# Kernel tuning notes

Measured on AMD Instinct MI355X. Metric: run time of the kernel, lower is better.

The kernel has to match this reference:

```python
import jax, jax.numpy as jnp
import numpy as np

N_NODES = 100000
N_EDGES = 800000
F_IN, N_HID, N_CLS = 256, 128, 40


def setup_inputs() -> dict:
    key = jax.random.key(0)
    ks = jax.random.split(key, 6)
    features = jax.random.normal(ks[0], (N_NODES, F_IN), dtype=jnp.float32)
    src = jax.random.randint(ks[1], (N_EDGES,), 0, N_NODES, dtype=jnp.int64)
    dst = jax.random.randint(ks[2], (N_EDGES,), 0, N_NODES, dtype=jnp.int64)
    W1 = jax.random.normal(ks[3], (F_IN, N_HID), dtype=jnp.float32) / np.sqrt(F_IN)
    b1 = jnp.zeros((N_HID,), dtype=jnp.float32)
    W2 = jax.random.normal(ks[4], (N_HID, N_CLS), dtype=jnp.float32) / np.sqrt(N_HID)
    b2 = jnp.zeros((N_CLS,), dtype=jnp.float32)
    return {"features": features, "src": src, "dst": dst,
            "W1": W1, "b1": b1, "W2": W2, "b2": b2}


def reference(features, src, dst, W1, b1, W2, b2):
    # DGL GraphConv with norm='both': h = D_dst^{-1/2} A (D_src^{-1/2} x) W + b
    # Eval mode: dropout(p=0.85) is identity.
    N = features.shape[0]
    ones = jnp.ones(src.shape[0], dtype=features.dtype)
    out_deg = jax.ops.segment_sum(ones, src, num_segments=N)
    in_deg = jax.ops.segment_sum(ones, dst, num_segments=N)
    norm_src = jnp.where(out_deg > 0, out_deg ** -0.5, 0.0)[:, None]  # [N,1]
    norm_dst = jnp.where(in_deg > 0, in_deg ** -0.5, 0.0)[:, None]

    def gconv(x, W, b):
        # project first (in_feats >= out_feats here) to shrink SpMM width
        h = (x * norm_src) @ W                                # [N, out]
        agg = jax.ops.segment_sum(h[src], dst, num_segments=N)  # sparse aggregate
        return agg * norm_dst + b

    x = jax.nn.relu(gconv(features, W1, b1))
    return gconv(x, W2, b2)
```

## Files before the change

kernel.cpp:

```cpp
#include <hip/hip_runtime.h>
#include <hip/hip_bf16.h>
#include <math.h>


#define F_IN  256
#define F_HID 128
#define F_CLS 40

#define RSZ 8192
#define NSL 32

typedef __bf16 bf16_t;
typedef bf16_t bf16x8 __attribute__((ext_vector_type(8)));
typedef float floatx4 __attribute__((ext_vector_type(4)));

static __device__ __forceinline__ unsigned short f2b(float f) {
    __hip_bfloat16 h = __float2bfloat16(f);
    return __builtin_bit_cast(unsigned short, h);
}
static __device__ __forceinline__ float b2f(unsigned short u) {
    return __uint_as_float((unsigned)u << 16);
}
static __device__ __forceinline__ unsigned short f2h(float f) {
    return __builtin_bit_cast(unsigned short, (_Float16)f);
}
static __device__ __forceinline__ float h2f(unsigned short u) {
    return (float)__builtin_bit_cast(_Float16, u);
}

__global__ __launch_bounds__(256) void hist_kernel(
    const int* __restrict__ src, const int* __restrict__ dst,
    unsigned* __restrict__ partial_s, unsigned* __restrict__ partial_d, int E)
{
    __shared__ unsigned h[RSZ];
    const int t = threadIdx.x;
    const int r  = blockIdx.x / NSL;
    const int sl = blockIdx.x % NSL;
    const int lo = r * RSZ;
    const int* __restrict__ keys = blockIdx.y ? dst : src;
    unsigned* __restrict__ part = blockIdx.y ? partial_d : partial_s;

    for (int i = t; i < RSZ; i += 256) h[i] = 0;
    __syncthreads();

    const int slice = (E + NSL - 1) / NSL;
    const int e0 = sl * slice;
    const int e1 = min(E, e0 + slice);

    int e = e0 + t;
    for (; e + 7 * 256 < e1; e += 8 * 256) {
        int k[8];
        #pragma unroll
        for (int i = 0; i < 8; ++i) k[i] = keys[e + i * 256];
        #pragma unroll
        for (int i = 0; i < 8; ++i) {
            unsigned kk = (unsigned)(k[i] - lo);
            if (kk < RSZ) atomicAdd(&h[kk], 1u);
        }
    }
    for (; e < e1; e += 256) {
        unsigned kk = (unsigned)(keys[e] - lo);
        if (kk < RSZ) atomicAdd(&h[kk], 1u);
    }
    __syncthreads();

    unsigned* dst_p = part + (size_t)blockIdx.x * RSZ;
    for (int i = t; i < RSZ; i += 256) dst_p[i] = h[i];
}

__global__ __launch_bounds__(256) void degnorm_kernel(
    const unsigned* __restrict__ partial_s, const unsigned* __restrict__ partial_d,
    int* __restrict__ cnt_dst, float* __restrict__ norm_src,
    float* __restrict__ norm_dst, int N)
{
    int i = blockIdx.x * 256 + threadIdx.x;
    if (i >= N) return;
    int r = i / RSZ;
    int off = i & (RSZ - 1);
    const unsigned* ps = partial_s + (size_t)r * NSL * RSZ + off;
    const unsigned* pd = partial_d + (size_t)r * NSL * RSZ + off;
    unsigned ss = 0, sd = 0;
    #pragma unroll
    for (int sl = 0; sl < NSL; ++sl) {
        ss += ps[(size_t)sl * RSZ];
        sd += pd[(size_t)sl * RSZ];
    }
    cnt_dst[i] = (int)sd;
    norm_src[i] = ss ? 1.0f / sqrtf((float)ss) : 0.0f;
    norm_dst[i] = sd ? 1.0f / sqrtf((float)sd) : 0.0f;
}

__global__ __launch_bounds__(256) void scan1_kernel(const int* __restrict__ cnt,
                                                    int* __restrict__ row_off,
                                                    int* __restrict__ blk_sums, int N) {
    __shared__ int s[256];
    const int t = threadIdx.x;
    const int base = blockIdx.x * 1024 + t * 4;
    int v0 = (base + 0 < N) ? cnt[base + 0] : 0;
    int v1 = (base + 1 < N) ? cnt[base + 1] : 0;
    int v2 = (base + 2 < N) ? cnt[base + 2] : 0;
    int v3 = (base + 3 < N) ? cnt[base + 3] : 0;
    int local = v0 + v1 + v2 + v3;
    s[t] = local;
    __syncthreads();
    for (int off = 1; off < 256; off <<= 1) {
        int x = (t >= off) ? s[t - off] : 0;
        __syncthreads();
        s[t] += x;
        __syncthreads();
    }
    int excl = s[t] - local;
    if (t == 255) blk_sums[blockIdx.x] = s[t];
    if (base + 0 < N) row_off[base + 0] = excl;
    if (base + 1 < N) row_off[base + 1] = excl + v0;
    if (base + 2 < N) row_off[base + 2] = excl + v0 + v1;
    if (base + 3 < N) row_off[base + 3] = excl + v0 + v1 + v2;
}

__global__ __launch_bounds__(256) void scan2_kernel(int* __restrict__ blk_sums, int B) {
    __shared__ int s[256];
    const int t = threadIdx.x;
    int local = (t < B) ? blk_sums[t] : 0;
    s[t] = local;
    __syncthreads();
    for (int off = 1; off < 256; off <<= 1) {
        int x = (t >= off) ? s[t - off] : 0;
        __syncthreads();
        s[t] += x;
        __syncthreads();
    }
    if (t < B) blk_sums[t] = s[t] - local;
}

__global__ __launch_bounds__(256) void scan3_kernel(int* __restrict__ row_off,
                                                    const int* __restrict__ blk_sums,
                                                    int N, int E) {
    const int t = threadIdx.x;
    const int base = blockIdx.x * 1024 + t * 4;
    const int add = blk_sums[blockIdx.x];
    #pragma unroll
    for (int i = 0; i < 4; ++i) {
        int idx = base + i;
        if (idx < N) row_off[idx] += add;
    }
    if (blockIdx.x == 0 && t == 0) row_off[N] = E;
}

__global__ __launch_bounds__(256) void slicepref_kernel(
    unsigned* __restrict__ partial_d, const int* __restrict__ row_off,
    int N, int NRtot)
{
    int idx = blockIdx.x * 256 + threadIdx.x;
    if (idx >= NRtot) return;
    int r = idx / RSZ;
    int i = idx & (RSZ - 1);
    unsigned run = (idx < N) ? (unsigned)row_off[idx] : 0u;
    unsigned* p = partial_d + (size_t)r * NSL * RSZ + i;
    #pragma unroll
    for (int sl = 0; sl < NSL; ++sl) {
        unsigned c = p[(size_t)sl * RSZ];
        p[(size_t)sl * RSZ] = run;
        run += c;
    }
}

__global__ __launch_bounds__(256) void scatter2_kernel(
    const int* __restrict__ src, const int* __restrict__ dst,
    const unsigned* __restrict__ pref, int* __restrict__ csr_src, int E)
{
    __shared__ unsigned cur[RSZ];
    const int t = threadIdx.x;
    const int r  = blockIdx.x / NSL;
    const int sl = blockIdx.x % NSL;
    const int lo = r * RSZ;
    const unsigned* p = pref + (size_t)blockIdx.x * RSZ;

    for (int i = t; i < RSZ; i += 256) cur[i] = p[i];
    __syncthreads();

    const int slice = (E + NSL - 1) / NSL;
    const int e0 = sl * slice;
    const int e1 = min(E, e0 + slice);

    int e = e0 + t;
    for (; e + 7 * 256 < e1; e += 8 * 256) {
        int d[8], s[8];
        #pragma unroll
        for (int i = 0; i < 8; ++i) { d[i] = dst[e + i * 256]; s[i] = src[e + i * 256]; }
        #pragma unroll
        for (int i = 0; i < 8; ++i) {
            unsigned k = (unsigned)(d[i] - lo);
            if (k < RSZ) {
                unsigned pos = atomicAdd(&cur[k], 1u);
                csr_src[pos] = s[i];
            }
        }
    }
    for (; e < e1; e += 256) {
        unsigned k = (unsigned)(dst[e] - lo);
        if (k < RSZ) {
            unsigned pos = atomicAdd(&cur[k], 1u);
            csr_src[pos] = src[e];
        }
    }
}

__global__ __launch_bounds__(256) void pack_w1t_kernel(const float* __restrict__ W1,
                                                       __hip_bfloat16* __restrict__ W1t) {
    int idx = blockIdx.x * 256 + threadIdx.x;
    int n = idx >> 8;
    int k = idx & 255;
    W1t[idx] = __float2bfloat16(W1[(size_t)k * F_HID + n]);
}

__global__ __launch_bounds__(512, 4) void gemm1_mfma_kernel(
    const float* __restrict__ X, const __hip_bfloat16* __restrict__ W1t,
    const float* __restrict__ norm_src, __hip_bfloat16* __restrict__ h1b, int N)
{
    __shared__ __hip_bfloat16 Bs[128 * 256];
    const int t = threadIdx.x;
    const int node0 = blockIdx.x * 128;
    const int lane = t & 63;
    const int w = t >> 6;
    const int l15 = lane & 15;
    const int quad = lane >> 4;

    const int arow = node0 + w * 16 + l15;
    const bool valid = arow < N;
    const int arow_c = valid ? arow : (N - 1);
    const float ns = valid ? norm_src[arow] : 0.0f;

    const float* xp = X + (size_t)arow_c * F_IN + quad * 8;

    float4 araw[4];
    araw[0] = *(const float4*)(xp + 0);
    araw[1] = *(const float4*)(xp + 4);
    araw[2] = *(const float4*)(xp + 32);
    araw[3] = *(const float4*)(xp + 36);

    #pragma unroll
    for (int i = 0; i < 8; ++i) {
        int idx = i * 512 + t;
        int row = idx >> 5;
        int ch  = idx & 31;
        uint4 v = *(const uint4*)(W1t + (size_t)row * F_IN + ch * 8);
        int d = row * 256 + ((ch * 8) ^ ((row & 7) << 3));
        *(uint4*)(Bs + d) = v;
    }
    __syncthreads();

    const int swz = (l15 & 7) << 3;
    const int bbase0 = l15 * 256 + ((quad * 8) ^ swz);
    const int bbase1 = l15 * 256 + ((32 + quad * 8) ^ swz);

    floatx4 acc[8] = {};

    #pragma unroll
    for (int c = 0; c < 4; ++c) {
        bf16x8 ab0, ab1;
        {
            union { bf16x8 v; unsigned short u[8]; } cv;
            cv.u[0] = f2b(araw[0].x * ns); cv.u[1] = f2b(araw[0].y * ns);
            cv.u[2] = f2b(araw[0].z * ns); cv.u[3] = f2b(araw[0].w * ns);
            cv.u[4] = f2b(araw[1].x * ns); cv.u[5] = f2b(araw[1].y * ns);
            cv.u[6] = f2b(araw[1].z * ns); cv.u[7] = f2b(araw[1].w * ns);
            ab0 = cv.v;
            cv.u[0] = f2b(araw[2].x * ns); cv.u[1] = f2b(araw[2].y * ns);
            cv.u[2] = f2b(araw[2].z * ns); cv.u[3] = f2b(araw[2].w * ns);
            cv.u[4] = f2b(araw[3].x * ns); cv.u[5] = f2b(araw[3].y * ns);
            cv.u[6] = f2b(araw[3].z * ns); cv.u[7] = f2b(araw[3].w * ns);
            ab1 = cv.v;
        }
        if (c < 3) {
            araw[0] = *(const float4*)(xp + (c + 1) * 64 + 0);
            araw[1] = *(const float4*)(xp + (c + 1) * 64 + 4);
            araw[2] = *(const float4*)(xp + (c + 1) * 64 + 32);
            araw[3] = *(const float4*)(xp + (c + 1) * 64 + 36);
        }
        #pragma unroll
        for (int nt = 0; nt < 8; ++nt) {
            bf16x8 b = *(const bf16x8*)(Bs + bbase0 + nt * 16 * 256 + c * 64);
            acc[nt] = __builtin_amdgcn_mfma_f32_16x16x32_bf16(ab0, b, acc[nt], 0, 0, 0);
        }
        #pragma unroll
        for (int nt = 0; nt < 8; ++nt) {
            bf16x8 b = *(const bf16x8*)(Bs + bbase1 + nt * 16 * 256 + c * 64);
            acc[nt] = __builtin_amdgcn_mfma_f32_16x16x32_bf16(ab1, b, acc[nt], 0, 0, 0);
        }
    }

    #pragma unroll
    for (int nt = 0; nt < 8; ++nt) {
        #pragma unroll
        for (int r = 0; r < 4; ++r) {
            int node = node0 + w * 16 + quad * 4 + r;
            if (node < N)
                h1b[(size_t)node * F_HID + nt * 16 + l15] = __float2bfloat16(acc[nt][r]);
        }
    }
}

__global__ __launch_bounds__(256) void spmm1_csr_kernel(
    const __hip_bfloat16* __restrict__ h1b, const int* __restrict__ row_off,
    const int* __restrict__ csr_src, const float* __restrict__ norm_src,
    const float* __restrict__ norm_dst, const float* __restrict__ b1,
    unsigned short* __restrict__ h1act, int N)
{
    const int t = threadIdx.x;
    const int node = blockIdx.x * 8 + (t >> 5);
    if (node >= N) return;
    const int c = (t & 31) << 2;
    const int start = row_off[node];
    const int end = row_off[node + 1];
    float4 acc = make_float4(0.f, 0.f, 0.f, 0.f);
    int j = start;
    for (; j + 8 <= end; j += 8) {
        int s[8];
        #pragma unroll
        for (int i = 0; i < 8; ++i) s[i] = csr_src[j + i];
        ushort4 u[8];
        #pragma unroll
        for (int i = 0; i < 8; ++i)
            u[i] = *(const ushort4*)(h1b + (size_t)s[i] * F_HID + c);
        #pragma unroll
        for (int i = 0; i < 8; ++i) {
            acc.x += b2f(u[i].x);
            acc.y += b2f(u[i].y);
            acc.z += b2f(u[i].z);
            acc.w += b2f(u[i].w);
        }
    }
    for (; j + 2 <= end; j += 2) {
        int s0 = csr_src[j + 0];
        int s1 = csr_src[j + 1];
        ushort4 u0 = *(const ushort4*)(h1b + (size_t)s0 * F_HID + c);
        ushort4 u1 = *(const ushort4*)(h1b + (size_t)s1 * F_HID + c);
        acc.x += b2f(u0.x) + b2f(u1.x);
        acc.y += b2f(u0.y) + b2f(u1.y);
        acc.z += b2f(u0.z) + b2f(u1.z);
        acc.w += b2f(u0.w) + b2f(u1.w);
    }
    if (j < end) {
        int s = csr_src[j];
        ushort4 u = *(const ushort4*)(h1b + (size_t)s * F_HID + c);
        acc.x += b2f(u.x);
        acc.y += b2f(u.y);
        acc.z += b2f(u.z);
        acc.w += b2f(u.w);
    }
    const float nd = norm_dst[node];
    const float ns = norm_src[node];
    float4 bb = *(const float4*)(b1 + c);
    ushort4 o;
    o.x = f2h(fmaxf(fmaf(acc.x, nd, bb.x), 0.f) * ns);
    o.y = f2h(fmaxf(fmaf(acc.y, nd, bb.y), 0.f) * ns);
    o.z = f2h(fmaxf(fmaf(acc.z, nd, bb.z), 0.f) * ns);
    o.w = f2h(fmaxf(fmaf(acc.w, nd, bb.w), 0.f) * ns);
    *(ushort4*)(h1act + (size_t)node * F_HID + c) = o;
}

__global__ __launch_bounds__(320) void gemm2_kernel(
    const unsigned short* __restrict__ h1act, const float* __restrict__ W2,
    unsigned short* __restrict__ h2, int N)
{
    __shared__ float As[64][132];
    __shared__ float Ws[128][40];
    const int t = threadIdx.x;
    const int node0 = blockIdx.x * 64;

    #pragma unroll
    for (int i = 0; i < 4; ++i) {
        int f = t + 320 * i;
        int r = f / 10;
        int kk = (f % 10) * 4;
        *(float4*)&Ws[r][kk] = *(const float4*)(W2 + (size_t)r * F_CLS + kk);
    }
    for (int f = t; f < 2048; f += 320) {
        int r = f >> 5;
        int kk = (f & 31) << 2;
        int node = node0 + r;
        float4 v = make_float4(0.f, 0.f, 0.f, 0.f);
        if (node < N) {
            ushort4 u = *(const ushort4*)(h1act + (size_t)node * F_HID + kk);
            v.x = h2f(u.x); v.y = h2f(u.y); v.z = h2f(u.z); v.w = h2f(u.w);
        }
        *(float4*)&As[r][kk] = v;
    }
    __syncthreads();

    const int col = t % 40;
    const int rowg = t / 40;
    float acc[8] = {};
    #pragma unroll 8
    for (int k = 0; k < F_HID; ++k) {
        float w = Ws[k][col];
        #pragma unroll
        for (int i = 0; i < 8; ++i)
            acc[i] = fmaf(As[rowg * 8 + i][k], w, acc[i]);
    }
    #pragma unroll
    for (int i = 0; i < 8; ++i) {
        int node = node0 + rowg * 8 + i;
        if (node < N) h2[(size_t)node * F_CLS + col] = f2h(acc[i]);
    }
}

__global__ __launch_bounds__(256) void spmm2_csr_kernel(
    const unsigned short* __restrict__ h2, const int* __restrict__ row_off,
    const int* __restrict__ csr_src, const float* __restrict__ norm_dst,
    const float* __restrict__ b2, float* __restrict__ out, int N)
{
    const int t = threadIdx.x;
    const int node = blockIdx.x * 16 + (t >> 4);
    const int lane = t & 15;
    if (node >= N || lane >= 10) return;
    const int c = lane << 2;
    const int start = row_off[node];
    const int end = row_off[node + 1];
    float4 acc = make_float4(0.f, 0.f, 0.f, 0.f);
    int j = start;
    for (; j + 8 <= end; j += 8) {
        int s[8];
        #pragma unroll
        for (int i = 0; i < 8; ++i) s[i] = csr_src[j + i];
        ushort4 u[8];
        #pragma unroll
        for (int i = 0; i < 8; ++i)
            u[i] = *(const ushort4*)(h2 + (size_t)s[i] * F_CLS + c);
        #pragma unroll
        for (int i = 0; i < 8; ++i) {
            acc.x += h2f(u[i].x);
            acc.y += h2f(u[i].y);
            acc.z += h2f(u[i].z);
            acc.w += h2f(u[i].w);
        }
    }
    for (; j + 2 <= end; j += 2) {
        int s0 = csr_src[j + 0];
        int s1 = csr_src[j + 1];
        ushort4 u0 = *(const ushort4*)(h2 + (size_t)s0 * F_CLS + c);
        ushort4 u1 = *(const ushort4*)(h2 + (size_t)s1 * F_CLS + c);
        acc.x += h2f(u0.x) + h2f(u1.x);
        acc.y += h2f(u0.y) + h2f(u1.y);
        acc.z += h2f(u0.z) + h2f(u1.z);
        acc.w += h2f(u0.w) + h2f(u1.w);
    }
    if (j < end) {
        int s = csr_src[j];
        ushort4 u = *(const ushort4*)(h2 + (size_t)s * F_CLS + c);
        acc.x += h2f(u.x);
        acc.y += h2f(u.y);
        acc.z += h2f(u.z);
        acc.w += h2f(u.w);
    }
    float nd = norm_dst[node];
    float4 bb = *(const float4*)(b2 + c);
    float4 r;
    r.x = fmaf(acc.x, nd, bb.x);
    r.y = fmaf(acc.y, nd, bb.y);
    r.z = fmaf(acc.z, nd, bb.z);
    r.w = fmaf(acc.w, nd, bb.w);
    *(float4*)(out + (size_t)node * F_CLS + c) = r;
}

extern "C" void kernel_launch(void* const* d_in, const int* in_sizes, int n_in,
                              void* d_out, int out_size, void* d_ws, size_t ws_size,
                              hipStream_t stream) {
    const float* X   = (const float*)d_in[0];
    const int*   src = (const int*)d_in[1];
    const int*   dst = (const int*)d_in[2];
    const float* W1  = (const float*)d_in[3];
    const float* b1  = (const float*)d_in[4];
    const float* W2  = (const float*)d_in[5];
    const float* b2  = (const float*)d_in[6];
    float* out = (float*)d_out;

    const int N = in_sizes[0] / F_IN;
    const int E = in_sizes[1];
    const int NB = (N + 1023) / 1024;
    const int NR = (N + RSZ - 1) / RSZ;
    const int NRtot = NR * RSZ;

    char* w = (char*)d_ws;
    int*   cnt_dst  = (int*)w;                      w += (size_t)N * 4;
    int*   row_off  = (int*)w;                      w += (size_t)(N + 4) * 4;
    int*   blk_sums = (int*)w;                      w += 256 * 4;
    int*   csr_src  = (int*)w;                      w += (size_t)E * 4;
    float* norm_src = (float*)w;                    w += (size_t)N * 4;
    float* norm_dst = (float*)w;                    w += (size_t)N * 4;
    unsigned short* h1act = (unsigned short*)w;     w += (size_t)N * F_HID * 2;
    unsigned short* h2    = (unsigned short*)w;     w += (size_t)N * F_CLS * 2;
    __hip_bfloat16* W1t = (__hip_bfloat16*)w;       w += (size_t)F_HID * F_IN * 2;
    __hip_bfloat16* h1b = (__hip_bfloat16*)w;       w += (size_t)N * F_HID * 2;
    unsigned* partial_s = (unsigned*)w;             w += (size_t)NR * NSL * RSZ * 4;
    unsigned* partial_d = (unsigned*)w;             w += (size_t)NR * NSL * RSZ * 4;

    hist_kernel<<<dim3(NR * NSL, 2), 256, 0, stream>>>(src, dst, partial_s, partial_d, E);
    degnorm_kernel<<<(N + 255) / 256, 256, 0, stream>>>(partial_s, partial_d,
                                                        cnt_dst, norm_src, norm_dst, N);

    scan1_kernel<<<NB, 256, 0, stream>>>(cnt_dst, row_off, blk_sums, N);
    scan2_kernel<<<1, 256, 0, stream>>>(blk_sums, NB);
    scan3_kernel<<<NB, 256, 0, stream>>>(row_off, blk_sums, N, E);

    slicepref_kernel<<<(NRtot + 255) / 256, 256, 0, stream>>>(partial_d, row_off, N, NRtot);
    scatter2_kernel<<<NR * NSL, 256, 0, stream>>>(src, dst, partial_d, csr_src, E);

    pack_w1t_kernel<<<(F_HID * F_IN) / 256, 256, 0, stream>>>(W1, W1t);

    gemm1_mfma_kernel<<<(N + 127) / 128, 512, 0, stream>>>(X, W1t, norm_src, h1b, N);

    spmm1_csr_kernel<<<(N + 7) / 8, 256, 0, stream>>>(h1b, row_off, csr_src,
                                                      norm_src, norm_dst, b1, h1act, N);

    gemm2_kernel<<<(N + 63) / 64, 320, 0, stream>>>(h1act, W2, h2, N);

    spmm2_csr_kernel<<<(N + 15) / 16, 256, 0, stream>>>(h2, row_off, csr_src, norm_dst, b2, out, N);
}
```

Measured before the change: 347.8 us.

## Fuse preprocessing kernels, resize histogram regions, repack spmm2 threads

```diff
diff --git a/kernel.cpp b/kernel.cpp
--- a/kernel.cpp
+++ b/kernel.cpp
@@ -7,8 +7,8 @@
 #define F_HID 128
 #define F_CLS 40
 
-#define RSZ 8192
-#define NSL 32
+#define RSZ 16384
+#define NSL 16
 
 typedef __bf16 bf16_t;
 typedef bf16_t bf16x8 __attribute__((ext_vector_type(8)));
@@ -68,38 +68,51 @@
     for (int i = t; i < RSZ; i += 256) dst_p[i] = h[i];
 }
 
-__global__ __launch_bounds__(256) void degnorm_kernel(
+__global__ __launch_bounds__(256) void scan1_kernel(
     const unsigned* __restrict__ partial_s, const unsigned* __restrict__ partial_d,
-    int* __restrict__ cnt_dst, float* __restrict__ norm_src,
-    float* __restrict__ norm_dst, int N)
-{
-    int i = blockIdx.x * 256 + threadIdx.x;
-    if (i >= N) return;
-    int r = i / RSZ;
-    int off = i & (RSZ - 1);
-    const unsigned* ps = partial_s + (size_t)r * NSL * RSZ + off;
-    const unsigned* pd = partial_d + (size_t)r * NSL * RSZ + off;
-    unsigned ss = 0, sd = 0;
-    #pragma unroll
-    for (int sl = 0; sl < NSL; ++sl) {
-        ss += ps[(size_t)sl * RSZ];
-        sd += pd[(size_t)sl * RSZ];
-    }
-    cnt_dst[i] = (int)sd;
-    norm_src[i] = ss ? 1.0f / sqrtf((float)ss) : 0.0f;
-    norm_dst[i] = sd ? 1.0f / sqrtf((float)sd) : 0.0f;
-}
-
-__global__ __launch_bounds__(256) void scan1_kernel(const int* __restrict__ cnt,
-                                                    int* __restrict__ row_off,
-                                                    int* __restrict__ blk_sums, int N) {
+    int* __restrict__ row_off, int* __restrict__ blk_sums,
+    float* __restrict__ norm_src, float* __restrict__ norm_dst, int N)
+{
     __shared__ int s[256];
     const int t = threadIdx.x;
     const int base = blockIdx.x * 1024 + t * 4;
-    int v0 = (base + 0 < N) ? cnt[base + 0] : 0;
-    int v1 = (base + 1 < N) ? cnt[base + 1] : 0;
-    int v2 = (base + 2 < N) ? cnt[base + 2] : 0;
-    int v3 = (base + 3 < N) ? cnt[base + 3] : 0;
+
+    unsigned ss0 = 0, ss1 = 0, ss2 = 0, ss3 = 0;
+    unsigned sd0 = 0, sd1 = 0, sd2 = 0, sd3 = 0;
+    {
+        const int r = base / RSZ;
+        const int off = base & (RSZ - 1);
+        const unsigned* ps = partial_s + (size_t)r * NSL * RSZ + off;
+        const unsigned* pd = partial_d + (size_t)r * NSL * RSZ + off;
+        #pragma unroll
+        for (int sl = 0; sl < NSL; ++sl) {
+            uint4 a = *(const uint4*)(ps + (size_t)sl * RSZ);
+            uint4 b = *(const uint4*)(pd + (size_t)sl * RSZ);
+            ss0 += a.x; ss1 += a.y; ss2 += a.z; ss3 += a.w;
+            sd0 += b.x; sd1 += b.y; sd2 += b.z; sd3 += b.w;
+        }
+    }
+    if (base + 0 < N) {
+        norm_src[base + 0] = ss0 ? 1.0f / sqrtf((float)ss0) : 0.0f;
+        norm_dst[base + 0] = sd0 ? 1.0f / sqrtf((float)sd0) : 0.0f;
+    }
+    if (base + 1 < N) {
+        norm_src[base + 1] = ss1 ? 1.0f / sqrtf((float)ss1) : 0.0f;
+        norm_dst[base + 1] = sd1 ? 1.0f / sqrtf((float)sd1) : 0.0f;
+    }
+    if (base + 2 < N) {
+        norm_src[base + 2] = ss2 ? 1.0f / sqrtf((float)ss2) : 0.0f;
+        norm_dst[base + 2] = sd2 ? 1.0f / sqrtf((float)sd2) : 0.0f;
+    }
+    if (base + 3 < N) {
+        norm_src[base + 3] = ss3 ? 1.0f / sqrtf((float)ss3) : 0.0f;
+        norm_dst[base + 3] = sd3 ? 1.0f / sqrtf((float)sd3) : 0.0f;
+    }
+
+    int v0 = (base + 0 < N) ? (int)sd0 : 0;
+    int v1 = (base + 1 < N) ? (int)sd1 : 0;
+    int v2 = (base + 2 < N) ? (int)sd2 : 0;
+    int v3 = (base + 3 < N) ? (int)sd3 : 0;
     int local = v0 + v1 + v2 + v3;
     s[t] = local;
     __syncthreads();
@@ -117,9 +130,19 @@
     if (base + 3 < N) row_off[base + 3] = excl + v0 + v1 + v2;
 }
 
-__global__ __launch_bounds__(256) void scan2_kernel(int* __restrict__ blk_sums, int B) {
+__global__ __launch_bounds__(256) void scan2_pack_kernel(
+    int* __restrict__ blk_sums, int B,
+    const float* __restrict__ W1, __hip_bfloat16* __restrict__ W1t)
+{
+    const int t = threadIdx.x;
+    if (blockIdx.x > 0) {
+        int idx = (blockIdx.x - 1) * 256 + t;
+        int n = idx >> 8;
+        int k = idx & 255;
+        W1t[idx] = __float2bfloat16(W1[(size_t)k * F_HID + n]);
+        return;
+    }
     __shared__ int s[256];
-    const int t = threadIdx.x;
     int local = (t < B) ? blk_sums[t] : 0;
     s[t] = local;
     __syncthreads();
@@ -132,29 +155,21 @@
     if (t < B) blk_sums[t] = s[t] - local;
 }
 
-__global__ __launch_bounds__(256) void scan3_kernel(int* __restrict__ row_off,
-                                                    const int* __restrict__ blk_sums,
-                                                    int N, int E) {
-    const int t = threadIdx.x;
-    const int base = blockIdx.x * 1024 + t * 4;
-    const int add = blk_sums[blockIdx.x];
-    #pragma unroll
-    for (int i = 0; i < 4; ++i) {
-        int idx = base + i;
-        if (idx < N) row_off[idx] += add;
-    }
-    if (blockIdx.x == 0 && t == 0) row_off[N] = E;
-}
-
-__global__ __launch_bounds__(256) void slicepref_kernel(
-    unsigned* __restrict__ partial_d, const int* __restrict__ row_off,
-    int N, int NRtot)
-{
-    int idx = blockIdx.x * 256 + threadIdx.x;
+__global__ __launch_bounds__(256) void scan3_slicepref_kernel(
+    int* __restrict__ row_off, const int* __restrict__ blk_sums,
+    unsigned* __restrict__ partial_d, int N, int E, int NRtot)
+{
+    const int idx = blockIdx.x * 256 + threadIdx.x;
     if (idx >= NRtot) return;
-    int r = idx / RSZ;
-    int i = idx & (RSZ - 1);
-    unsigned run = (idx < N) ? (unsigned)row_off[idx] : 0u;
+    unsigned run = 0;
+    if (idx < N) {
+        int v = row_off[idx] + blk_sums[idx >> 10];
+        row_off[idx] = v;
+        run = (unsigned)v;
+    }
+    if (idx == N) row_off[N] = E;
+    const int r = idx / RSZ;
+    const int i = idx & (RSZ - 1);
     unsigned* p = partial_d + (size_t)r * NSL * RSZ + i;
     #pragma unroll
     for (int sl = 0; sl < NSL; ++sl) {
@@ -203,14 +218,6 @@
             csr_src[pos] = src[e];
         }
     }
-}
-
-__global__ __launch_bounds__(256) void pack_w1t_kernel(const float* __restrict__ W1,
-                                                       __hip_bfloat16* __restrict__ W1t) {
-    int idx = blockIdx.x * 256 + threadIdx.x;
-    int n = idx >> 8;
-    int k = idx & 255;
-    W1t[idx] = __float2bfloat16(W1[(size_t)k * F_HID + n]);
 }
 
 __global__ __launch_bounds__(512, 4) void gemm1_mfma_kernel(
@@ -411,9 +418,10 @@
     const float* __restrict__ b2, float* __restrict__ out, int N)
 {
     const int t = threadIdx.x;
-    const int node = blockIdx.x * 16 + (t >> 4);
-    const int lane = t & 15;
-    if (node >= N || lane >= 10) return;
+    if (t >= 250) return;
+    const int node = blockIdx.x * 25 + t / 10;
+    const int lane = t % 10;
+    if (node >= N) return;
     const int c = lane << 2;
     const int start = row_off[node];
     const int end = row_off[node + 1];
@@ -482,7 +490,6 @@
     const int NRtot = NR * RSZ;
 
     char* w = (char*)d_ws;
-    int*   cnt_dst  = (int*)w;                      w += (size_t)N * 4;
     int*   row_off  = (int*)w;                      w += (size_t)(N + 4) * 4;
     int*   blk_sums = (int*)w;                      w += 256 * 4;
     int*   csr_src  = (int*)w;                      w += (size_t)E * 4;
@@ -496,17 +503,14 @@
     unsigned* partial_d = (unsigned*)w;             w += (size_t)NR * NSL * RSZ * 4;
 
     hist_kernel<<<dim3(NR * NSL, 2), 256, 0, stream>>>(src, dst, partial_s, partial_d, E);
-    degnorm_kernel<<<(N + 255) / 256, 256, 0, stream>>>(partial_s, partial_d,
-                                                        cnt_dst, norm_src, norm_dst, N);
-
-    scan1_kernel<<<NB, 256, 0, stream>>>(cnt_dst, row_off, blk_sums, N);
-    scan2_kernel<<<1, 256, 0, stream>>>(blk_sums, NB);
-    scan3_kernel<<<NB, 256, 0, stream>>>(row_off, blk_sums, N, E);
-
-    slicepref_kernel<<<(NRtot + 255) / 256, 256, 0, stream>>>(partial_d, row_off, N, NRtot);
+
+    scan1_kernel<<<NB, 256, 0, stream>>>(partial_s, partial_d, row_off, blk_sums,
+                                         norm_src, norm_dst, N);
+    scan2_pack_kernel<<<1 + (F_HID * F_IN) / 256, 256, 0, stream>>>(blk_sums, NB, W1, W1t);
+    scan3_slicepref_kernel<<<(NRtot + 255) / 256, 256, 0, stream>>>(
+        row_off, blk_sums, partial_d, N, E, NRtot);
+
     scatter2_kernel<<<NR * NSL, 256, 0, stream>>>(src, dst, partial_d, csr_src, E);
-
-    pack_w1t_kernel<<<(F_HID * F_IN) / 256, 256, 0, stream>>>(W1, W1t);
 
     gemm1_mfma_kernel<<<(N + 127) / 128, 512, 0, stream>>>(X, W1t, norm_src, h1b, N);
 
@@ -515,5 +519,5 @@
 
     gemm2_kernel<<<(N + 63) / 64, 320, 0, stream>>>(h1act, W2, h2, N);
 
-    spmm2_csr_kernel<<<(N + 15) / 16, 256, 0, stream>>>(h2, row_off, csr_src, norm_dst, b2, out, N);
-}
+    spmm2_csr_kernel<<<(N + 24) / 25, 256, 0, stream>>>(h2, row_off, csr_src, norm_dst, b2, out, N);
+}
```

After: 352.1 us. About the same (+1.2%).
